# Kernel optimization log

Hardware: AMD Instinct MI355X
Metric: run time of the kernel (lower is better)

## Reference

```python
import jax, jax.numpy as jnp
import numpy as np

B, S, D_IN = 1, 2048, 2048
H, KV, HD = 32, 8, 64          # num_heads, num_kv_groups, head_dim
GS = H // KV                    # group_size
D_OUT = H * HD
EPS = 1e-6


def _rmsnorm(x, w):
    # RMSNormQwen over last dim (head_dim)
    var = jnp.mean(x * x, axis=-1, keepdims=True)
    return x * jax.lax.rsqrt(var + EPS) * w


def _rope(x, cos, sin):
    # rotate-half RoPE; x: [B, heads, S, HD], cos/sin: [S, HD]
    d = x.shape[-1]
    x1, x2 = x[..., : d // 2], x[..., d // 2 :]
    rot = jnp.concatenate([-x2, x1], axis=-1)
    return x * cos + rot * sin


def setup_inputs() -> dict:
    key = jax.random.key(0)
    ks = jax.random.split(key, 8)
    x = jax.random.normal(ks[0], (B, S, D_IN), dtype=jnp.float32)
    Wq = jax.random.normal(ks[1], (D_IN, D_OUT), dtype=jnp.float32) * 0.02
    Wk = jax.random.normal(ks[2], (D_IN, KV * HD), dtype=jnp.float32) * 0.02
    Wv = jax.random.normal(ks[3], (D_IN, KV * HD), dtype=jnp.float32) * 0.02
    Wo = jax.random.normal(ks[4], (D_OUT, D_IN), dtype=jnp.float32) * 0.02
    q_norm_w = jnp.ones((HD,), dtype=jnp.float32)
    k_norm_w = jnp.ones((HD,), dtype=jnp.float32)
    # causal mask: True where masked (j > i)
    mask = jnp.triu(jnp.ones((S, S), dtype=bool), k=1)
    # RoPE tables
    inv_freq = 1.0 / (10000.0 ** (np.arange(0, HD, 2, dtype=np.float32) / HD))
    ang = np.arange(S, dtype=np.float32)[:, None] * inv_freq[None, :]  # [S, HD/2]
    cos = jnp.asarray(np.concatenate([np.cos(ang), np.cos(ang)], axis=-1))
    sin = jnp.asarray(np.concatenate([np.sin(ang), np.sin(ang)], axis=-1))
    return {"x": x, "mask": mask, "cos": cos, "sin": sin,
            "Wq": Wq, "Wk": Wk, "Wv": Wv, "Wo": Wo,
            "q_norm_w": q_norm_w, "k_norm_w": k_norm_w}


def reference(x, mask, cos, sin, Wq, Wk, Wv, Wo, q_norm_w, k_norm_w):
    b, s, _ = x.shape
    q = (x @ Wq).reshape(b, s, H, HD).transpose(0, 2, 1, 3)   # [B,H,S,HD]
    k = (x @ Wk).reshape(b, s, KV, HD).transpose(0, 2, 1, 3)  # [B,KV,S,HD]
    v = (x @ Wv).reshape(b, s, KV, HD).transpose(0, 2, 1, 3)  # [B,KV,S,HD]
    q = _rmsnorm(q, q_norm_w)
    k = _rmsnorm(k, k_norm_w)
    q = _rope(q, cos, sin)
    k = _rope(k, cos, sin)
    # grouped-KV attention without materializing repeated K/V
    qg = q.reshape(b, KV, GS, s, HD)
    scores = jnp.einsum('bkgsd,bktd->bkgst', qg, k)           # [B,KV,GS,S,S]
    scores = jnp.where(mask, -jnp.inf, scores)
    weights = jax.nn.softmax(scores / (HD ** 0.5), axis=-1)
    ctx = jnp.einsum('bkgst,bktd->bkgsd', weights, v)         # [B,KV,GS,S,HD]
    ctx = ctx.reshape(b, H, s, HD).transpose(0, 2, 1, 3).reshape(b, s, D_OUT)
    return ctx @ Wo
```

## Files before the change

### kernel.cpp

```cpp
#include <hip/hip_runtime.h>
#include <hip/hip_bf16.h>
#include <math.h>

#define S_LEN 2048
#define DIN   2048
#define NH    32
#define NKV   8
#define HD    64
#define DOUT  2048
#define QKVN  3072
#define KOFF  2048
#define VOFF  2560

typedef __attribute__((ext_vector_type(8))) short short8v;
typedef __attribute__((ext_vector_type(8))) unsigned short ushort8v;
typedef __attribute__((ext_vector_type(4))) unsigned short ushort4v;
typedef __attribute__((ext_vector_type(4))) float float4v;

__device__ __forceinline__ float bf2f(unsigned short u) {
    union { float f; unsigned u; } c; c.u = ((unsigned)u) << 16; return c.f;
}
__device__ __forceinline__ unsigned short f2bf(float f) {
    union { float f; unsigned u; } c; c.f = f;
    unsigned r = c.u + 0x7fffu + ((c.u >> 16) & 1u);
    return (unsigned short)(r >> 16);
}
__device__ __forceinline__ unsigned short f2h(float f) {
    union { _Float16 h; unsigned short u; } c; c.h = (_Float16)f; return c.u;
}
__device__ __forceinline__ float h2f(unsigned short u) {
    union { _Float16 h; unsigned short u; } c; c.u = u; return (float)c.h;
}

__global__ __launch_bounds__(256) void prep(const float* __restrict__ Wq,
                                            const float* __restrict__ Wk,
                                            const float* __restrict__ Wv,
                                            const float* __restrict__ Wo,
                                            const float* __restrict__ x,
                                            unsigned short* __restrict__ W1,
                                            unsigned short* __restrict__ WoT,
                                            unsigned short* __restrict__ XB) {
    __shared__ float t[32][33];
    const int a = blockIdx.x;
    const int tx = threadIdx.x & 31, ty = threadIdx.x >> 5;
    if (a < 6144) {
        const int n0 = (a % 96) * 32, k0 = (a / 96) * 32;
        const float* src; int nn0, Nsrc;
        if (n0 < KOFF)      { src = Wq; nn0 = n0;        Nsrc = DOUT; }
        else if (n0 < VOFF) { src = Wk; nn0 = n0 - KOFF; Nsrc = 512; }
        else                { src = Wv; nn0 = n0 - VOFF; Nsrc = 512; }
#pragma unroll
        for (int j = ty; j < 32; j += 8)
            t[j][tx] = src[(size_t)(k0 + j) * Nsrc + nn0 + tx];
        __syncthreads();
#pragma unroll
        for (int j = ty; j < 32; j += 8)
            W1[(size_t)(n0 + j) * DIN + k0 + tx] = f2bf(t[tx][j]);
    } else if (a < 10240) {
        const int b = a - 6144;
        const int n0 = (b % 64) * 32, k0 = (b / 64) * 32;
#pragma unroll
        for (int j = ty; j < 32; j += 8)
            t[j][tx] = Wo[(size_t)(k0 + j) * DIN + n0 + tx];
        __syncthreads();
#pragma unroll
        for (int j = ty; j < 32; j += 8)
            WoT[(size_t)(n0 + j) * DOUT + k0 + tx] = f2bf(t[tx][j]);
    } else {
        const int i = (a - 10240) * 1024 + threadIdx.x * 4;
        float4 v = *(const float4*)(x + i);
        XB[i + 0] = f2bf(v.x); XB[i + 1] = f2bf(v.y);
        XB[i + 2] = f2bf(v.z); XB[i + 3] = f2bf(v.w);
    }
}

template <int FUSE>
__global__ __launch_bounds__(256) void gemm64(const unsigned short* __restrict__ A,
                                              const unsigned short* __restrict__ Bt,
                                              void* __restrict__ Cv, int M, int N, int K,
                                              const float* __restrict__ qnw,
                                              const float* __restrict__ knw,
                                              const float* __restrict__ cosb,
                                              const float* __restrict__ sinb) {
    __shared__ __attribute__((aligned(16))) unsigned short As[128 * 32];
    __shared__ __attribute__((aligned(16))) unsigned short Bs[64 * 32];
    const int tid = threadIdx.x, lane = tid & 63, w = tid >> 6;
    const int bm = blockIdx.y * 128, bn = blockIdx.x * 64;
    const int wm = w * 32;

    float4v acc[2][4];
#pragma unroll
    for (int i = 0; i < 2; i++)
#pragma unroll
        for (int j = 0; j < 4; j++) acc[i][j] = (float4v){0.f, 0.f, 0.f, 0.f};

    const int lr = lane >> 2, lc = (lane & 3) * 8;
    const unsigned short* Ag0 = A + (size_t)(bm + w * 32 + lr) * K + lc;
    const unsigned short* Ag1 = Ag0 + (size_t)16 * K;
    const unsigned short* Bg  = Bt + (size_t)(bn + w * 16 + lr) * K + lc;
    unsigned short* Al0 = As + (w * 32) * 32;
    unsigned short* Al1 = As + (w * 32 + 16) * 32;
    unsigned short* Bl  = Bs + (w * 16) * 32;

    const int frow = lane & 15, fk = (lane >> 4) * 8;

    for (int k0 = 0; k0 < K; k0 += 32) {
        __syncthreads();
        __builtin_amdgcn_global_load_lds(
            (const __attribute__((address_space(1))) void*)(Ag0 + k0),
            (__attribute__((address_space(3))) void*)Al0, 16, 0, 0);
        __builtin_amdgcn_global_load_lds(
            (const __attribute__((address_space(1))) void*)(Ag1 + k0),
            (__attribute__((address_space(3))) void*)Al1, 16, 0, 0);
        __builtin_amdgcn_global_load_lds(
            (const __attribute__((address_space(1))) void*)(Bg + k0),
            (__attribute__((address_space(3))) void*)Bl, 16, 0, 0);
        __syncthreads();

        short8v af[2], bf[4];
#pragma unroll
        for (int fm = 0; fm < 2; fm++)
            af[fm] = *(const short8v*)(As + (wm + fm * 16 + frow) * 32 + fk);
#pragma unroll
        for (int fn = 0; fn < 4; fn++)
            bf[fn] = *(const short8v*)(Bs + (fn * 16 + frow) * 32 + fk);
#pragma unroll
        for (int fm = 0; fm < 2; fm++)
#pragma unroll
            for (int fn = 0; fn < 4; fn++)
                acc[fm][fn] = __builtin_amdgcn_mfma_f32_16x16x32_bf16(
                    af[fm], bf[fn], acc[fm][fn], 0, 0, 0);
    }

    const int quad = lane >> 4, col16 = lane & 15;
    if constexpr (FUSE == 1) {
        unsigned short* C = (unsigned short*)Cv;
        const int head = bn >> 6;
        if (head < 40) {
            const float* nw = (head < 32) ? qnw : knw;
            float wv[4];
#pragma unroll
            for (int fn = 0; fn < 4; fn++) wv[fn] = nw[fn * 16 + col16];
#pragma unroll
            for (int fm = 0; fm < 2; fm++)
#pragma unroll
                for (int r = 0; r < 4; r++) {
                    float x0 = acc[fm][0][r], x1 = acc[fm][1][r];
                    float x2 = acc[fm][2][r], x3 = acc[fm][3][r];
                    float ss = x0 * x0 + x1 * x1 + x2 * x2 + x3 * x3;
                    ss += __shfl_xor(ss, 1); ss += __shfl_xor(ss, 2);
                    ss += __shfl_xor(ss, 4); ss += __shfl_xor(ss, 8);
                    const float inv = rsqrtf(ss * (1.0f / 64.0f) + 1e-6f);
                    float xn[4] = {x0 * inv * wv[0], x1 * inv * wv[1],
                                   x2 * inv * wv[2], x3 * inv * wv[3]};
                    const int row = bm + wm + fm * 16 + quad * 4 + r;
                    const float* cr = cosb + (size_t)row * HD;
                    const float* sr = sinb + (size_t)row * HD;
#pragma unroll
                    for (int fn = 0; fn < 4; fn++) {
                        const float rot = (fn < 2) ? -xn[fn + 2] : xn[fn - 2];
                        const float res = xn[fn] * cr[fn * 16 + col16] +
                                          rot * sr[fn * 16 + col16];
                        C[(size_t)row * N + bn + fn * 16 + col16] = f2bf(res);
                    }
                }
        } else {
#pragma unroll
            for (int fm = 0; fm < 2; fm++)
#pragma unroll
                for (int fn = 0; fn < 4; fn++)
#pragma unroll
                    for (int r = 0; r < 4; r++)
                        C[(size_t)(bm + wm + fm * 16 + quad * 4 + r) * N +
                          bn + fn * 16 + col16] = f2bf(acc[fm][fn][r]);
        }
    } else {
        float* C = (float*)Cv;
#pragma unroll
        for (int fm = 0; fm < 2; fm++)
#pragma unroll
            for (int fn = 0; fn < 4; fn++)
#pragma unroll
                for (int r = 0; r < 4; r++)
                    C[(size_t)(bm + wm + fm * 16 + quad * 4 + r) * N +
                      bn + fn * 16 + col16] = acc[fm][fn][r];
    }
}

#define KSTR 88
#define PPSTR 72

__global__ __launch_bounds__(256) void flash_part(const unsigned short* __restrict__ qb,
                                                  const unsigned short* __restrict__ kb,
                                                  const unsigned short* __restrict__ vb,
                                                  unsigned short* __restrict__ Op,
                                                  float* __restrict__ Lp) {
    __shared__ __attribute__((aligned(16))) unsigned short Ks[64 * KSTR];
    __shared__ __attribute__((aligned(16))) unsigned short Vt[64 * KSTR];
    __shared__ __attribute__((aligned(16))) unsigned short Ps[128 * PPSTR];

    const int tid = threadIdx.x, lane = tid & 63, w = tid >> 6;
    const int col = lane & 15, quad = lane >> 4;
    const int bid = blockIdx.x;
    const int g = bid & 7;
    const int qtile = (bid >> 3) & 63;
    const int half = bid >> 9;
    const int s0 = qtile * 32;
    const int h = g * 4 + w;

    const int nt = (s0 + 95) >> 6;
    const int nt0 = (nt + 1) >> 1;
    const int it_lo = half ? nt0 : 0;
    const int it_hi = half ? nt : nt0;

    const float C1 = 0.18033688011112042f;
    const float C2 = 12.262908856239697f;

    unsigned short* Oh = Op + (size_t)half * S_LEN * DOUT;
    float* Lh = Lp + (size_t)half * S_LEN * NKV * 4;

    short8v qf[2][2];
#pragma unroll
    for (int mf = 0; mf < 2; mf++)
#pragma unroll
        for (int ks = 0; ks < 2; ks++)
            qf[mf][ks] = *(const short8v*)(qb + (size_t)(s0 + mf * 16 + col) * QKVN +
                                           h * HD + ks * 32 + quad * 8);

    float4v O[2][4];
    float lsum[2][4];
#pragma unroll
    for (int mf = 0; mf < 2; mf++) {
#pragma unroll
        for (int df = 0; df < 4; df++) O[mf][df] = (float4v){0.f, 0.f, 0.f, 0.f};
#pragma unroll
        for (int r = 0; r < 4; r++) lsum[mf][r] = 0.f;
    }

    const int kkey = tid >> 2, kch = tid & 3;
    const unsigned short* kg = kb + (size_t)kkey * QKVN + g * HD + kch * 16;
    const int vkey = tid & 63, vdb = tid >> 6;
    const unsigned short* vg = vb + (size_t)vkey * QKVN + g * HD + vdb * 16;

    const size_t p0 = (size_t)it_lo * 64 * QKVN;
    ushort8v ka0 = *(const ushort8v*)(kg + p0);
    ushort8v ka1 = *(const ushort8v*)(kg + p0 + 8);
    ushort8v va0 = *(const ushort8v*)(vg + p0);
    ushort8v va1 = *(const ushort8v*)(vg + p0 + 8);

    for (int it = it_lo; it < it_hi; it++) {
        if (it > it_lo) __syncthreads();
        {
            unsigned short* kd = Ks + kkey * KSTR + kch * 16;
            *(ushort8v*)kd = ka0;
            *(ushort8v*)(kd + 8) = ka1;
            unsigned short* vd = Vt + (size_t)(vdb * 16) * KSTR + vkey;
#pragma unroll
            for (int j = 0; j < 8; j++) vd[j * KSTR] = va0[j];
#pragma unroll
            for (int j = 0; j < 8; j++) vd[(8 + j) * KSTR] = va1[j];
        }
        __syncthreads();
        if (it + 1 < it_hi) {
            const size_t off = (size_t)(it + 1) * 64 * QKVN;
            ka0 = *(const ushort8v*)(kg + off);
            ka1 = *(const ushort8v*)(kg + off + 8);
            va0 = *(const ushort8v*)(vg + off);
            va1 = *(const ushort8v*)(vg + off + 8);
        }

        const int t0 = it * 64;
        const bool edge = (t0 + 63 > s0);

        short8v kf[4][2];
#pragma unroll
        for (int nf = 0; nf < 4; nf++)
#pragma unroll
            for (int ks = 0; ks < 2; ks++)
                kf[nf][ks] = *(const short8v*)(Ks + (nf * 16 + col) * KSTR +
                                               ks * 32 + quad * 8);

#pragma unroll
        for (int mf = 0; mf < 2; mf++) {
            float4v sc[4];
#pragma unroll
            for (int nf = 0; nf < 4; nf++) {
                sc[nf] = (float4v){0.f, 0.f, 0.f, 0.f};
#pragma unroll
                for (int ks = 0; ks < 2; ks++)
                    sc[nf] = __builtin_amdgcn_mfma_f32_16x16x32_bf16(qf[mf][ks], kf[nf][ks],
                                                                     sc[nf], 0, 0, 0);
            }
#pragma unroll
            for (int nf = 0; nf < 4; nf++)
#pragma unroll
                for (int r = 0; r < 4; r++) {
                    float arg = sc[nf][r] * C1 - C2;
                    if (edge) {
                        const int qg = s0 + mf * 16 + quad * 4 + r;
                        const int kg_ = t0 + nf * 16 + col;
                        arg = (kg_ <= qg) ? arg : -100.f;
                    }
                    const float p = exp2f(arg);
                    sc[nf][r] = p;
                    lsum[mf][r] += p;
                }
            unsigned short* pw = Ps + (size_t)(w * 32 + mf * 16 + quad * 4) * PPSTR;
#pragma unroll
            for (int nf = 0; nf < 4; nf++) {
                const int pb = (nf ^ quad) * 16;
#pragma unroll
                for (int r = 0; r < 4; r++)
                    pw[r * PPSTR + pb + col] = f2bf(sc[nf][r]);
            }
        }

        short8v vf[4][2];
#pragma unroll
        for (int df = 0; df < 4; df++)
#pragma unroll
            for (int ks = 0; ks < 2; ks++)
                vf[df][ks] = *(const short8v*)(Vt + (df * 16 + col) * KSTR +
                                               ks * 32 + quad * 8);
#pragma unroll
        for (int mf = 0; mf < 2; mf++)
#pragma unroll
            for (int ks = 0; ks < 2; ks++) {
                const int lb = ks * 2 + (quad >> 1);
                short8v pf = *(const short8v*)(Ps + (size_t)(w * 32 + mf * 16 + col) * PPSTR +
                                               ((lb ^ (col >> 2)) * 16 + (quad & 1) * 8));
#pragma unroll
                for (int df = 0; df < 4; df++)
                    O[mf][df] = __builtin_amdgcn_mfma_f32_16x16x32_bf16(pf, vf[df][ks],
                                                                        O[mf][df], 0, 0, 0);
            }
    }

#pragma unroll
    for (int mf = 0; mf < 2; mf++)
#pragma unroll
        for (int r = 0; r < 4; r++) {
            float l = lsum[mf][r];
            l += __shfl_xor(l, 1); l += __shfl_xor(l, 2);
            l += __shfl_xor(l, 4); l += __shfl_xor(l, 8);
            if (col == 0)
                Lh[(size_t)(s0 + mf * 16 + quad * 4 + r) * NH + h] = l;
        }
#pragma unroll
    for (int mf = 0; mf < 2; mf++)
#pragma unroll
        for (int df = 0; df < 4; df++)
#pragma unroll
            for (int r = 0; r < 4; r++)
                Oh[(size_t)(s0 + mf * 16 + quad * 4 + r) * DOUT + h * HD + df * 16 + col] =
                    f2h(O[mf][df][r]);
}

__global__ __launch_bounds__(256) void combine(unsigned short* O01,
                                               const float* __restrict__ Lp) {
    const int i4 = (blockIdx.x * 256 + threadIdx.x) * 4;
    const int s = i4 >> 11, h = (i4 & 2047) >> 6;
    const float inv = 1.0f / (Lp[(size_t)s * NH + h] +
                              Lp[(size_t)S_LEN * NH + (size_t)s * NH + h]);
    ushort4v o0 = *(const ushort4v*)(O01 + i4);
    ushort4v o1 = *(const ushort4v*)(O01 + (size_t)S_LEN * DOUT + i4);
    ushort4v r;
#pragma unroll
    for (int j = 0; j < 4; j++) r[j] = f2bf((h2f(o0[j]) + h2f(o1[j])) * inv);
    *(ushort4v*)(O01 + i4) = r;
}

extern "C" void kernel_launch(void* const* d_in, const int* in_sizes, int n_in,
                              void* d_out, int out_size, void* d_ws, size_t ws_size,
                              hipStream_t stream) {
    const float* x    = (const float*)d_in[0];
    const float* cosb = (const float*)d_in[2];
    const float* sinb = (const float*)d_in[3];
    const float* Wq   = (const float*)d_in[4];
    const float* Wk   = (const float*)d_in[5];
    const float* Wv   = (const float*)d_in[6];
    const float* Wo   = (const float*)d_in[7];
    const float* qw   = (const float*)d_in[8];
    const float* kw   = (const float*)d_in[9];
    float* out = (float*)d_out;

    unsigned short* W1  = (unsigned short*)d_ws;
    unsigned short* XB  = W1 + (size_t)QKVN * DIN;
    unsigned short* WoT = XB + (size_t)S_LEN * DIN;
    unsigned short* QKV = WoT + (size_t)DIN * DOUT;
    unsigned short* Op  = (unsigned short*)d_ws;
    float*          Lp  = (float*)(Op + (size_t)2 * S_LEN * DOUT);
    unsigned short* CTX = Op;

    dim3 blk256(256);

    prep<<<dim3(14336), blk256, 0, stream>>>(Wq, Wk, Wv, Wo, x, W1, WoT, XB);

    gemm64<1><<<dim3(QKVN / 64, S_LEN / 128), blk256, 0, stream>>>(
        XB, W1, QKV, S_LEN, QKVN, DIN, qw, kw, cosb, sinb);

    flash_part<<<dim3((S_LEN / 32) * NKV * 2), blk256, 0, stream>>>(
        QKV, QKV + KOFF, QKV + VOFF, Op, Lp);

    combine<<<dim3(S_LEN * DOUT / 1024), blk256, 0, stream>>>(Op, Lp);

    gemm64<0><<<dim3(DIN / 64, S_LEN / 128), blk256, 0, stream>>>(
        CTX, WoT, out, S_LEN, DIN, DOUT, nullptr, nullptr, nullptr, nullptr);
}
```

Measured before the change: 279.0 us.

## Use 32x32 MFMA with register-resident P and paired causal tile scheduling

The flash attention kernel moves from 16x16x32 to 32x32x16 bf16 MFMA and computes S^T so that P stays in registers. P is packed with v_cvt_pk_bf16_f32 and exchanged across the wave halves by lane shuffles, which removes the P round trip through shared memory. Work is rebalanced by pairing a short query tile with its long mirror tile in each block, so every block does about 17 key tiles. Only long tiles are split across the two partial outputs, and combine reads the second partial only for rows in the upper half. This cuts LDS traffic and load imbalance at the cost of more register pressure and a more complex per-block schedule.

Measured after the change: 264.8 us. 1.05x faster.

```diff
diff --git a/kernel.cpp b/kernel.cpp
--- a/kernel.cpp
+++ b/kernel.cpp
@@ -16,6 +16,7 @@
 typedef __attribute__((ext_vector_type(8))) unsigned short ushort8v;
 typedef __attribute__((ext_vector_type(4))) unsigned short ushort4v;
 typedef __attribute__((ext_vector_type(4))) float float4v;
+typedef __attribute__((ext_vector_type(16))) float float16v;
 
 __device__ __forceinline__ float bf2f(unsigned short u) {
     union { float f; unsigned u; } c; c.u = ((unsigned)u) << 16; return c.f;
@@ -30,6 +31,11 @@
 }
 __device__ __forceinline__ float h2f(unsigned short u) {
     union { _Float16 h; unsigned short u; } c; c.u = u; return (float)c.h;
+}
+__device__ __forceinline__ unsigned cvtpk(float lo, float hi) {
+    unsigned r;
+    asm("v_cvt_pk_bf16_f32 %0, %1, %2" : "=v"(r) : "v"(lo), "v"(hi));
+    return r;
 }
 
 __global__ __launch_bounds__(256) void prep(const float* __restrict__ Wq,
@@ -188,7 +194,6 @@
 }
 
 #define KSTR 88
-#define PPSTR 72
 
 __global__ __launch_bounds__(256) void flash_part(const unsigned short* __restrict__ qb,
                                                   const unsigned short* __restrict__ kb,
@@ -197,176 +202,179 @@
                                                   float* __restrict__ Lp) {
     __shared__ __attribute__((aligned(16))) unsigned short Ks[64 * KSTR];
     __shared__ __attribute__((aligned(16))) unsigned short Vt[64 * KSTR];
-    __shared__ __attribute__((aligned(16))) unsigned short Ps[128 * PPSTR];
 
     const int tid = threadIdx.x, lane = tid & 63, w = tid >> 6;
-    const int col = lane & 15, quad = lane >> 4;
+    const int sl = lane & 31, hi = lane >> 5, hi8 = hi * 8;
     const int bid = blockIdx.x;
     const int g = bid & 7;
-    const int qtile = (bid >> 3) & 63;
-    const int half = bid >> 9;
-    const int s0 = qtile * 32;
+    const int p = (bid >> 3) & 31;
+    const int s = bid >> 8;
     const int h = g * 4 + w;
 
-    const int nt = (s0 + 95) >> 6;
-    const int nt0 = (nt + 1) >> 1;
-    const int it_lo = half ? nt0 : 0;
-    const int it_hi = half ? nt : nt0;
+    const int s0a = p * 32, s0b = (63 - p) * 32;
+    const int nta = (s0a + 95) >> 6;
+    const int nA  = s ? 0 : nta;
+    const int bLo = s ? (17 - nta) : 0;
+    const int nB  = s ? 16 : (17 - nta);
+    const int nT  = nA + nB;
 
     const float C1 = 0.18033688011112042f;
     const float C2 = 12.262908856239697f;
 
-    unsigned short* Oh = Op + (size_t)half * S_LEN * DOUT;
-    float* Lh = Lp + (size_t)half * S_LEN * NKV * 4;
-
-    short8v qf[2][2];
-#pragma unroll
-    for (int mf = 0; mf < 2; mf++)
-#pragma unroll
-        for (int ks = 0; ks < 2; ks++)
-            qf[mf][ks] = *(const short8v*)(qb + (size_t)(s0 + mf * 16 + col) * QKVN +
-                                           h * HD + ks * 32 + quad * 8);
-
-    float4v O[2][4];
-    float lsum[2][4];
-#pragma unroll
-    for (int mf = 0; mf < 2; mf++) {
-#pragma unroll
-        for (int df = 0; df < 4; df++) O[mf][df] = (float4v){0.f, 0.f, 0.f, 0.f};
-#pragma unroll
-        for (int r = 0; r < 4; r++) lsum[mf][r] = 0.f;
-    }
+    unsigned short* Oh = Op + (size_t)s * S_LEN * DOUT;
+    float* Lh = Lp + (size_t)s * S_LEN * NH;
+
+    int s0 = nA ? s0a : s0b;
+
+    short8v qf[4];
+#pragma unroll
+    for (int ksq = 0; ksq < 4; ksq++)
+        qf[ksq] = *(const short8v*)(qb + (size_t)(s0 + sl) * QKVN + h * HD +
+                                    ksq * 16 + hi8);
+
+    float16v O[2];
+#pragma unroll
+    for (int df = 0; df < 2; df++)
+#pragma unroll
+        for (int r = 0; r < 16; r++) O[df][r] = 0.f;
+    float lsum = 0.f;
 
     const int kkey = tid >> 2, kch = tid & 3;
     const unsigned short* kg = kb + (size_t)kkey * QKVN + g * HD + kch * 16;
     const int vkey = tid & 63, vdb = tid >> 6;
     const unsigned short* vg = vb + (size_t)vkey * QKVN + g * HD + vdb * 16;
 
-    const size_t p0 = (size_t)it_lo * 64 * QKVN;
+    auto epi = [&](int sbase) {
+        float lt = lsum + __shfl_xor(lsum, 32);
+        if (hi == 0) Lh[(size_t)(sbase + sl) * NH + h] = lt;
+#pragma unroll
+        for (int df = 0; df < 2; df++)
+#pragma unroll
+            for (int r = 0; r < 16; r++) {
+                const int row = sbase + (r & 3) + 8 * (r >> 2) + 4 * hi;
+                Oh[(size_t)row * DOUT + h * HD + df * 32 + sl] = f2h(O[df][r]);
+            }
+    };
+
+    const int it0 = nA ? 0 : bLo;
+    const size_t p0 = (size_t)it0 * 64 * QKVN;
     ushort8v ka0 = *(const ushort8v*)(kg + p0);
     ushort8v ka1 = *(const ushort8v*)(kg + p0 + 8);
     ushort8v va0 = *(const ushort8v*)(vg + p0);
     ushort8v va1 = *(const ushort8v*)(vg + p0 + 8);
 
-    for (int it = it_lo; it < it_hi; it++) {
-        if (it > it_lo) __syncthreads();
+    for (int j = 0; j < nT; j++) {
+        if (j > 0) __syncthreads();
         {
             unsigned short* kd = Ks + kkey * KSTR + kch * 16;
             *(ushort8v*)kd = ka0;
             *(ushort8v*)(kd + 8) = ka1;
             unsigned short* vd = Vt + (size_t)(vdb * 16) * KSTR + vkey;
 #pragma unroll
-            for (int j = 0; j < 8; j++) vd[j * KSTR] = va0[j];
-#pragma unroll
-            for (int j = 0; j < 8; j++) vd[(8 + j) * KSTR] = va1[j];
+            for (int jj = 0; jj < 8; jj++) vd[jj * KSTR] = va0[jj];
+#pragma unroll
+            for (int jj = 0; jj < 8; jj++) vd[(8 + jj) * KSTR] = va1[jj];
         }
         __syncthreads();
-        if (it + 1 < it_hi) {
-            const size_t off = (size_t)(it + 1) * 64 * QKVN;
+        if (j + 1 < nT) {
+            const int itn = (j + 1 < nA) ? (j + 1) : (bLo + (j + 1 - nA));
+            const size_t off = (size_t)itn * 64 * QKVN;
             ka0 = *(const ushort8v*)(kg + off);
             ka1 = *(const ushort8v*)(kg + off + 8);
             va0 = *(const ushort8v*)(vg + off);
             va1 = *(const ushort8v*)(vg + off + 8);
         }
-
+        if (nA && j == nA) {
+            epi(s0a);
+#pragma unroll
+            for (int df = 0; df < 2; df++)
+#pragma unroll
+                for (int r = 0; r < 16; r++) O[df][r] = 0.f;
+            lsum = 0.f;
+            s0 = s0b;
+#pragma unroll
+            for (int ksq = 0; ksq < 4; ksq++)
+                qf[ksq] = *(const short8v*)(qb + (size_t)(s0b + sl) * QKVN +
+                                            h * HD + ksq * 16 + hi8);
+        }
+
+        const int it = (j < nA) ? j : (bLo + (j - nA));
         const int t0 = it * 64;
         const bool edge = (t0 + 63 > s0);
 
-        short8v kf[4][2];
-#pragma unroll
-        for (int nf = 0; nf < 4; nf++)
-#pragma unroll
-            for (int ks = 0; ks < 2; ks++)
-                kf[nf][ks] = *(const short8v*)(Ks + (nf * 16 + col) * KSTR +
-                                               ks * 32 + quad * 8);
-
-#pragma unroll
-        for (int mf = 0; mf < 2; mf++) {
-            float4v sc[4];
-#pragma unroll
-            for (int nf = 0; nf < 4; nf++) {
-                sc[nf] = (float4v){0.f, 0.f, 0.f, 0.f};
-#pragma unroll
-                for (int ks = 0; ks < 2; ks++)
-                    sc[nf] = __builtin_amdgcn_mfma_f32_16x16x32_bf16(qf[mf][ks], kf[nf][ks],
-                                                                     sc[nf], 0, 0, 0);
+#pragma unroll
+        for (int b = 0; b < 2; b++) {
+            short8v kf[4];
+#pragma unroll
+            for (int ksq = 0; ksq < 4; ksq++)
+                kf[ksq] = *(const short8v*)(Ks + (32 * b + sl) * KSTR +
+                                            ksq * 16 + hi8);
+            float16v sct;
+#pragma unroll
+            for (int r = 0; r < 16; r++) sct[r] = 0.f;
+#pragma unroll
+            for (int ksq = 0; ksq < 4; ksq++)
+                sct = __builtin_amdgcn_mfma_f32_32x32x16_bf16(kf[ksq], qf[ksq],
+                                                              sct, 0, 0, 0);
+#pragma unroll
+            for (int r = 0; r < 16; r++) {
+                float arg = sct[r] * C1 - C2;
+                if (edge) {
+                    const int kglob = t0 + 32 * b + (r & 3) + 8 * (r >> 2) + 4 * hi;
+                    arg = (kglob <= s0 + sl) ? arg : -100.f;
+                }
+                const float pv = exp2f(arg);
+                sct[r] = pv;
+                lsum += pv;
             }
-#pragma unroll
-            for (int nf = 0; nf < 4; nf++)
-#pragma unroll
-                for (int r = 0; r < 4; r++) {
-                    float arg = sc[nf][r] * C1 - C2;
-                    if (edge) {
-                        const int qg = s0 + mf * 16 + quad * 4 + r;
-                        const int kg_ = t0 + nf * 16 + col;
-                        arg = (kg_ <= qg) ? arg : -100.f;
-                    }
-                    const float p = exp2f(arg);
-                    sc[nf][r] = p;
-                    lsum[mf][r] += p;
+            unsigned pk[8];
+#pragma unroll
+            for (int i = 0; i < 8; i++) pk[i] = cvtpk(sct[2 * i], sct[2 * i + 1]);
+#pragma unroll
+            for (int kk = 0; kk < 2; kk++) {
+                const unsigned x0 = pk[4 * kk + 0], x1 = pk[4 * kk + 1];
+                const unsigned y0 = pk[4 * kk + 2], y1 = pk[4 * kk + 3];
+                const unsigned a0 = __shfl_xor(x0, 32), a1 = __shfl_xor(x1, 32);
+                const unsigned b0 = __shfl_xor(y0, 32), b1 = __shfl_xor(y1, 32);
+                union { unsigned u[4]; short8v v; } pa;
+                pa.u[0] = hi ? b0 : x0;
+                pa.u[1] = hi ? b1 : x1;
+                pa.u[2] = hi ? y0 : a0;
+                pa.u[3] = hi ? y1 : a1;
+                const int ks = 2 * b + kk;
+#pragma unroll
+                for (int df = 0; df < 2; df++) {
+                    const short8v vf = *(const short8v*)(Vt + (size_t)(df * 32 + sl) * KSTR +
+                                                         ks * 16 + hi8);
+                    O[df] = __builtin_amdgcn_mfma_f32_32x32x16_bf16(pa.v, vf,
+                                                                    O[df], 0, 0, 0);
                 }
-            unsigned short* pw = Ps + (size_t)(w * 32 + mf * 16 + quad * 4) * PPSTR;
-#pragma unroll
-            for (int nf = 0; nf < 4; nf++) {
-                const int pb = (nf ^ quad) * 16;
-#pragma unroll
-                for (int r = 0; r < 4; r++)
-                    pw[r * PPSTR + pb + col] = f2bf(sc[nf][r]);
             }
         }
-
-        short8v vf[4][2];
-#pragma unroll
-        for (int df = 0; df < 4; df++)
-#pragma unroll
-            for (int ks = 0; ks < 2; ks++)
-                vf[df][ks] = *(const short8v*)(Vt + (df * 16 + col) * KSTR +
-                                               ks * 32 + quad * 8);
-#pragma unroll
-        for (int mf = 0; mf < 2; mf++)
-#pragma unroll
-            for (int ks = 0; ks < 2; ks++) {
-                const int lb = ks * 2 + (quad >> 1);
-                short8v pf = *(const short8v*)(Ps + (size_t)(w * 32 + mf * 16 + col) * PPSTR +
-                                               ((lb ^ (col >> 2)) * 16 + (quad & 1) * 8));
-#pragma unroll
-                for (int df = 0; df < 4; df++)
-                    O[mf][df] = __builtin_amdgcn_mfma_f32_16x16x32_bf16(pf, vf[df][ks],
-                                                                        O[mf][df], 0, 0, 0);
-            }
     }
 
-#pragma unroll
-    for (int mf = 0; mf < 2; mf++)
-#pragma unroll
-        for (int r = 0; r < 4; r++) {
-            float l = lsum[mf][r];
-            l += __shfl_xor(l, 1); l += __shfl_xor(l, 2);
-            l += __shfl_xor(l, 4); l += __shfl_xor(l, 8);
-            if (col == 0)
-                Lh[(size_t)(s0 + mf * 16 + quad * 4 + r) * NH + h] = l;
-        }
-#pragma unroll
-    for (int mf = 0; mf < 2; mf++)
-#pragma unroll
-        for (int df = 0; df < 4; df++)
-#pragma unroll
-            for (int r = 0; r < 4; r++)
-                Oh[(size_t)(s0 + mf * 16 + quad * 4 + r) * DOUT + h * HD + df * 16 + col] =
-                    f2h(O[mf][df][r]);
+    epi(s0);
 }
 
 __global__ __launch_bounds__(256) void combine(unsigned short* O01,
                                                const float* __restrict__ Lp) {
     const int i4 = (blockIdx.x * 256 + threadIdx.x) * 4;
-    const int s = i4 >> 11, h = (i4 & 2047) >> 6;
-    const float inv = 1.0f / (Lp[(size_t)s * NH + h] +
-                              Lp[(size_t)S_LEN * NH + (size_t)s * NH + h]);
+    const int srow = i4 >> 11, hh = (i4 & 2047) >> 6;
+    float l = Lp[(size_t)srow * NH + hh];
     ushort4v o0 = *(const ushort4v*)(O01 + i4);
-    ushort4v o1 = *(const ushort4v*)(O01 + (size_t)S_LEN * DOUT + i4);
+    float acc[4];
+#pragma unroll
+    for (int j = 0; j < 4; j++) acc[j] = h2f(o0[j]);
+    if (srow >= 1024) {
+        l += Lp[(size_t)S_LEN * NH + (size_t)srow * NH + hh];
+        ushort4v o1 = *(const ushort4v*)(O01 + (size_t)S_LEN * DOUT + i4);
+#pragma unroll
+        for (int j = 0; j < 4; j++) acc[j] += h2f(o1[j]);
+    }
+    const float inv = 1.0f / l;
     ushort4v r;
 #pragma unroll
-    for (int j = 0; j < 4; j++) r[j] = f2bf((h2f(o0[j]) + h2f(o1[j])) * inv);
+    for (int j = 0; j < 4; j++) r[j] = f2bf(acc[j] * inv);
     *(ushort4v*)(O01 + i4) = r;
 }
 
@@ -399,7 +407,7 @@
     gemm64<1><<<dim3(QKVN / 64, S_LEN / 128), blk256, 0, stream>>>(
         XB, W1, QKV, S_LEN, QKVN, DIN, qw, kw, cosb, sinb);
 
-    flash_part<<<dim3((S_LEN / 32) * NKV * 2), blk256, 0, stream>>>(
+    flash_part<<<dim3(NKV * 32 * 2), blk256, 0, stream>>>(
         QKV, QKV + KOFF, QKV + VOFF, Op, Lp);
 
     combine<<<dim3(S_LEN * DOUT / 1024), blk256, 0, stream>>>(Op, Lp);
```
